# Kernel tuning notes

Measured on AMD Instinct MI355X. Metric: run time of the kernel, lower is better.

Reference implementation:

```python
import jax, jax.numpy as jnp
import numpy as np

B, S, D, H = 2, 2048, 1024, 16
HD = D // H  # 64


def setup_inputs() -> dict:
    key = jax.random.key(0)
    k0, k1, k2 = jax.random.split(key, 3)
    return {
        "x": jax.random.normal(k0, (B, S, D), jnp.float32),
        "qkv_w": jax.random.normal(k1, (D, 3 * D), jnp.float32) / np.sqrt(D).astype(np.float32),
        "qkv_b": jnp.zeros((3 * D,), jnp.float32),
        "out_w": jax.random.normal(k2, (D, D), jnp.float32) / np.sqrt(D).astype(np.float32),
        "out_b": jnp.zeros((D,), jnp.float32),
    }


def reference(x, qkv_w, qkv_b, out_w, out_b):
    b, s, d = x.shape
    h, hd = H, d // H
    scale = 1.0 / np.sqrt(hd).astype(np.float32)
    # qkv projection: [b, s, 3d] -> [b, s, 3, h, hd]
    qkv = (x @ qkv_w + qkv_b).reshape(b, s, 3, h, hd)
    q, k, v = qkv[:, :, 0], qkv[:, :, 1], qkv[:, :, 2]  # each [b, s, h, hd]
    # attention logits [b, h, q, k]
    logits = jnp.einsum("bqhd,bkhd->bhqk", q, k)
    # causal mask applied before scaling (as in source; -inf is scale-invariant)
    causal_mask = jnp.triu(jnp.ones((s, s), bool), 1)
    logits = jnp.where(causal_mask, -jnp.inf, logits) * scale
    att = jax.nn.softmax(logits, axis=-1)
    out = jnp.einsum("bhqk,bkhd->bqhd", att, v).reshape(b, s, d)
    return out @ out_w + out_b
```

## Files before the change

### kernel.cpp

```cpp
#include <hip/hip_runtime.h>


typedef __bf16 bf16x8 __attribute__((ext_vector_type(8)));
typedef float f32x4 __attribute__((ext_vector_type(4)));
typedef float f32x16 __attribute__((ext_vector_type(16)));
typedef unsigned short u16;
typedef u16 u16x8 __attribute__((ext_vector_type(8)));
typedef unsigned u32x4 __attribute__((ext_vector_type(4)));

#define NEG_INF (-__builtin_inff())
#define QSCALE 0.180336880110323f
#define FIXED_M 24.0f

__device__ __forceinline__ u16 f2b(float f) {
    unsigned u = __builtin_bit_cast(unsigned, f);
    u += 0x7fffu + ((u >> 16) & 1u);
    return (u16)(u >> 16);
}

__device__ __forceinline__ unsigned cvtpk(float lo, float hi) {
    unsigned r;
    asm("v_cvt_pk_bf16_f32 %0, %1, %2" : "=v"(r) : "v"(lo), "v"(hi));
    return r;
}

__device__ __forceinline__ void plswap(unsigned &a, unsigned &b) {
    asm("v_permlane32_swap_b32 %0, %1" : "+v"(a), "+v"(b));
}

__device__ __forceinline__ void gload_lds16(const u16* g, u16* l) {
    __builtin_amdgcn_global_load_lds(
        (__attribute__((address_space(1))) unsigned int*)(g),
        (__attribute__((address_space(3))) unsigned int*)(l),
        16u, 0, 0u);
}

__device__ __forceinline__ int swzb(int u) {
    return u ^ (((u >> 7) & 7) << 4);
}

__global__ void cast_f32_bf16(const float* __restrict__ X, u16* __restrict__ Y, int n4)
{
    int i = blockIdx.x * blockDim.x + threadIdx.x;
    if (i >= n4) return;
    float4 v = ((const float4*)X)[i];
    ((ushort4*)Y)[i] = make_ushort4(f2b(v.x), f2b(v.y), f2b(v.z), f2b(v.w));
}

__global__ void transpose_cast(const float* __restrict__ W, u16* __restrict__ Wt, int K, int N)
{
    __shared__ float tile[32][33];
    const int c0 = blockIdx.x * 32, r0 = blockIdx.y * 32;
    const int tc = threadIdx.x & 31, tr = threadIdx.x >> 5;
#pragma unroll
    for (int i = 0; i < 4; ++i)
        tile[tr + i*8][tc] = W[(size_t)(r0 + tr + i*8) * N + c0 + tc];
    __syncthreads();
#pragma unroll
    for (int i = 0; i < 4; ++i) {
        int nn = tr + i*8;
        Wt[(size_t)(c0 + nn) * K + r0 + tc] = f2b(tile[tc][nn]);
    }
}

template<int MODE>
__global__ __launch_bounds__(256) void gemm_bt(
    const u16* __restrict__ A, const u16* __restrict__ Bt,
    const float* __restrict__ bias, float* __restrict__ Cf,
    u16* __restrict__ qb, u16* __restrict__ kb, u16* __restrict__ vb,
    int M, int N, int K)
{
    __shared__ __align__(16) u16 As[2][128 * 32];
    __shared__ __align__(16) u16 Bs[2][128 * 32];
    const int tid  = threadIdx.x;
    const int wave = tid >> 6, lane = tid & 63;
    const int quad = lane >> 4, l16 = lane & 15;
    const int m0 = blockIdx.y * 128, n0 = blockIdx.x * 128;
    const int wm = (wave >> 1) * 64, wn = (wave & 1) * 64;

    f32x4 acc[4][4] = {};

    auto stage = [&](int buf, int kt) {
#pragma unroll
        for (int iss = 0; iss < 2; ++iss) {
            const int e = iss * 2048 + tid * 8;
            const int row = e >> 5, col = e & 31;
            gload_lds16(A  + (size_t)(m0 + row) * K + kt + col, &As[buf][iss * 2048 + wave * 512]);
            gload_lds16(Bt + (size_t)(n0 + row) * K + kt + col, &Bs[buf][iss * 2048 + wave * 512]);
        }
    };

    stage(0, 0);
    __syncthreads();

    int buf = 0;
    for (int kt = 0; kt < K; kt += 32) {
        if (kt + 32 < K) stage(buf ^ 1, kt + 32);

        bf16x8 af[4], bfr[4];
#pragma unroll
        for (int i = 0; i < 4; ++i) {
            af[i]  = *(const bf16x8*)(&As[buf][(wm + i*16 + l16) * 32 + quad * 8]);
            bfr[i] = *(const bf16x8*)(&Bs[buf][(wn + i*16 + l16) * 32 + quad * 8]);
        }
#pragma unroll
        for (int i = 0; i < 4; ++i)
#pragma unroll
            for (int j = 0; j < 4; ++j)
                acc[i][j] = __builtin_amdgcn_mfma_f32_16x16x32_bf16(af[i], bfr[j], acc[i][j], 0, 0, 0);
        __syncthreads();
        buf ^= 1;
    }

#pragma unroll
    for (int i = 0; i < 4; ++i)
#pragma unroll
        for (int j = 0; j < 4; ++j)
#pragma unroll
            for (int r = 0; r < 4; ++r) {
                const int m = m0 + wm + i*16 + quad*4 + r;
                const int n = n0 + wn + j*16 + l16;
                float v = acc[i][j][r] + bias[n];
                if (MODE == 0) {
                    Cf[(size_t)m * N + n] = v;
                } else {
                    const int t = n >> 10, h = (n >> 6) & 15, hd = n & 63;
                    const int b = m >> 11, s = m & 2047;
                    const size_t idx = ((size_t)(b * 16 + h) * 2048 + s) * 64 + hd;
                    if (t == 0)      qb[idx] = f2b(v * QSCALE);
                    else if (t == 1) kb[idx] = f2b(v);
                    else             vb[idx] = f2b(v);
                }
            }
}

__global__ __launch_bounds__(256) void transpose_v(const u16* __restrict__ vb, u16* __restrict__ vt)
{
    __shared__ u16 tile[64][72];
    const int bh = blockIdx.y, s0 = blockIdx.x * 64;
    const size_t base = (size_t)bh * (2048 * 64);
    const int r = threadIdx.x >> 3, c = (threadIdx.x & 7) * 8;
#pragma unroll
    for (int i = 0; i < 2; ++i) {
        u16x8 v = *(const u16x8*)(vb + base + (size_t)(s0 + r + i*32) * 64 + c);
        *(u16x8*)(&tile[r + i*32][c]) = v;
    }
    __syncthreads();
#pragma unroll
    for (int i = 0; i < 2; ++i) {
        const int hd = r + i*32;
        u16 tmp[8];
#pragma unroll
        for (int j = 0; j < 8; ++j) tmp[j] = tile[c + j][hd];
        *(u16x8*)(vt + base + (size_t)hd * 2048 + s0 + c) = *(u16x8*)&tmp[0];
    }
}

__global__ __launch_bounds__(256) void flash_attn(
    const u16* __restrict__ qb, const u16* __restrict__ kb, const u16* __restrict__ vt,
    u16* __restrict__ attn)
{
    __shared__ __align__(16) u16 Kl[2][4096];
    __shared__ __align__(16) u16 Vl[2][4096];
    __shared__ float red_f[2][2][2][16][64];
    __shared__ float red_li[2][2][64];
    __shared__ float al[2][2][32];

    const int tid  = threadIdx.x;
    const int wave = tid >> 6, lane = tid & 63;
    const int l31 = lane & 31, hi = lane >> 5;
    const int hi8 = hi * 8, hi4 = hi * 4;

    const int lin = (int)blockIdx.x;
    const int bh  = (lin & 7) | (((lin >> 3) & 3) << 3);
    const int g   = lin >> 5;
    const int pairsel = wave >> 1, phase = wave & 1;
    const int p   = 2 * g + pairsel;
    const size_t base = (size_t)bh * (2048 * 64);

    const int rb0 = 32 * p;
    const int rb1 = 32 * (63 - p);
    const int klo = p, khi = 63 - p;
    const int T = 32 - g;

    int koff[2], voff[2], dstw[2];
#pragma unroll
    for (int i = 0; i < 2; ++i) {
        const int u = (tid + 256 * i) * 16;
        const int ktsub = u >> 12, krow = (u >> 7) & 31;
        koff[i] = (ktsub * 32 + krow) * 64 + ((u & 127) >> 1);
        const int half = (u >> 6) & 1;
        voff[i] = (krow * 2 + half) * 2048 + ktsub * 32 + ((u & 63) >> 1);
        dstw[i] = swzb(u) >> 1;
    }
    int rdK[4], rdV[2][2];
#pragma unroll
    for (int ks = 0; ks < 4; ++ks) {
        const int u = phase * 4096 + l31 * 128 + ks * 32 + hi * 16;
        rdK[ks] = swzb(u) >> 1;
    }
#pragma unroll
    for (int c = 0; c < 2; ++c)
#pragma unroll
        for (int s2 = 0; s2 < 2; ++s2) {
            const int u = phase * 4096 + (c * 16 + (l31 >> 1)) * 128 + (l31 & 1) * 64
                        + s2 * 32 + hi * 16;
            rdV[c][s2] = swzb(u) >> 1;
        }

    bf16x8 qf[2][4];
#pragma unroll
    for (int ks = 0; ks < 4; ++ks) {
        qf[0][ks] = *(const bf16x8*)(qb + base + (size_t)(rb0 + l31) * 64 + ks*16 + hi8);
        qf[1][ks] = *(const bf16x8*)(qb + base + (size_t)(rb1 + l31) * 64 + ks*16 + hi8);
    }

    f32x16 minit;
#pragma unroll
    for (int r = 0; r < 16; ++r) minit[r] = -FIXED_M;

    f32x16 of[2][2] = {};
    float li[2] = {0.f, 0.f};

    u16x8 rk[2], rv[2];
    auto LOADS = [&](int s) {
#pragma unroll
        for (int i = 0; i < 2; ++i) {
            rk[i] = *(const u16x8*)(kb + base + (size_t)s * 4096 + koff[i]);
            rv[i] = *(const u16x8*)(vt + base + (size_t)s * 64 + voff[i]);
        }
    };
    auto WRITES = [&](int b) {
#pragma unroll
        for (int i = 0; i < 2; ++i) {
            *(u16x8*)(&Kl[b][dstw[i]]) = rk[i];
            *(u16x8*)(&Vl[b][dstw[i]]) = rv[i];
        }
    };

    LOADS(0); WRITES(0);
    __syncthreads();

    for (int s = 0; s < T; ++s) {
        const bool pre = (s + 1 < T);
        if (pre) LOADS(s + 1);

        const int kth = 2 * s + phase;
        const int key0 = kth * 32;
        const bool a_hi = (kth <= khi), a_lo = (kth <= klo);

        if (a_hi | a_lo) {
            const int buf = s & 1;
            bf16x8 kf[4], vf[2][2];
#pragma unroll
            for (int ks = 0; ks < 4; ++ks)
                kf[ks] = *(const bf16x8*)(&Kl[buf][rdK[ks]]);
#pragma unroll
            for (int c = 0; c < 2; ++c)
#pragma unroll
                for (int s2 = 0; s2 < 2; ++s2)
                    vf[c][s2] = *(const bf16x8*)(&Vl[buf][rdV[c][s2]]);

#define PROC_TILE(TT, RB, MT)                                                    \
        do {                                                                     \
            __builtin_amdgcn_s_setprio(1);                                       \
            f32x16 st = __builtin_amdgcn_mfma_f32_32x32x16_bf16(kf[0], qf[TT][0], minit, 0, 0, 0); \
            _Pragma("unroll")                                                    \
            for (int ks = 1; ks < 4; ++ks)                                       \
                st = __builtin_amdgcn_mfma_f32_32x32x16_bf16(kf[ks], qf[TT][ks], st, 0, 0, 0); \
            __builtin_amdgcn_s_setprio(0);                                       \
            const bool mt_ = (MT);                                               \
            const int lim_ = (RB) + l31 - key0;                                  \
            _Pragma("unroll")                                                    \
            for (int r = 0; r < 16; ++r) {                                       \
                float e = __builtin_exp2f(st[r]);                                \
                if (mt_ && ((r&3) + 8*(r>>2) + hi4 > lim_)) e = 0.f;             \
                st[r] = e;                                                       \
            }                                                                    \
            li[TT] += (((st[0]+st[1]) + (st[2]+st[3])) + ((st[4]+st[5]) + (st[6]+st[7]))) \
                    + (((st[8]+st[9]) + (st[10]+st[11])) + ((st[12]+st[13]) + (st[14]+st[15]))); \
            unsigned cw[8];                                                      \
            _Pragma("unroll")                                                    \
            for (int i = 0; i < 8; ++i) cw[i] = cvtpk(st[2*i], st[2*i+1]);       \
            plswap(cw[0], cw[2]); plswap(cw[1], cw[3]);                          \
            plswap(cw[4], cw[6]); plswap(cw[5], cw[7]);                          \
            bf16x8 pa[2];                                                        \
            { u32x4 t0 = {cw[0], cw[1], cw[2], cw[3]};                           \
              u32x4 t1 = {cw[4], cw[5], cw[6], cw[7]};                           \
              pa[0] = __builtin_bit_cast(bf16x8, t0);                            \
              pa[1] = __builtin_bit_cast(bf16x8, t1); }                          \
            __builtin_amdgcn_s_setprio(1);                                       \
            _Pragma("unroll")                                                    \
            for (int c = 0; c < 2; ++c) {                                        \
                of[TT][c] = __builtin_amdgcn_mfma_f32_32x32x16_bf16(pa[0], vf[c][0], of[TT][c], 0, 0, 0); \
                of[TT][c] = __builtin_amdgcn_mfma_f32_32x32x16_bf16(pa[1], vf[c][1], of[TT][c], 0, 0, 0); \
            }                                                                    \
            __builtin_amdgcn_s_setprio(0);                                       \
        } while (0)

            if (a_hi) PROC_TILE(1, rb1, kth == khi);
            if (a_lo) PROC_TILE(0, rb0, kth == klo);
#undef PROC_TILE
        }

        if (pre) WRITES((s + 1) & 1);
        __syncthreads();
    }

    if (phase) {
#pragma unroll
        for (int t = 0; t < 2; ++t) {
#pragma unroll
            for (int c = 0; c < 2; ++c)
#pragma unroll
                for (int i = 0; i < 16; ++i)
                    red_f[pairsel][t][c][i][lane] = of[t][c][i];
            red_li[pairsel][t][lane] = li[t];
        }
    }
    __syncthreads();
    if (phase) return;
#pragma unroll
    for (int t = 0; t < 2; ++t) {
#pragma unroll
        for (int c = 0; c < 2; ++c)
#pragma unroll
            for (int i = 0; i < 16; ++i)
                of[t][c][i] += red_f[pairsel][t][c][i][lane];
        li[t] += red_li[pairsel][t][lane];
    }

#pragma unroll
    for (int t = 0; t < 2; ++t) {
        li[t] += __shfl_xor(li[t], 32);
        al[pairsel][t][l31] = li[t];
    }
    const int b = bh >> 4, h = bh & 15;
    const int rbs[2] = {rb0, rb1};
#pragma unroll
    for (int t = 0; t < 2; ++t)
#pragma unroll
        for (int gq = 0; gq < 4; ++gq) {
            const f32x4 lv = *(const f32x4*)(&al[pairsel][t][gq*8 + hi4]);
            f32x4 inv;
#pragma unroll
            for (int rr = 0; rr < 4; ++rr) inv[rr] = 1.0f / lv[rr];
#pragma unroll
            for (int c = 0; c < 2; ++c)
#pragma unroll
                for (int rr = 0; rr < 4; ++rr) {
                    const int q = rbs[t] + gq*8 + hi4 + rr;
                    u16* dst = attn + ((size_t)(b * 2048 + q)) * 1024 + h * 64 + c*32;
                    dst[l31] = f2b(of[t][c][gq*4 + rr] * inv[rr]);
                }
        }
}

extern "C" void kernel_launch(void* const* d_in, const int* in_sizes, int n_in,
                              void* d_out, int out_size, void* d_ws, size_t ws_size,
                              hipStream_t stream)
{
    const float* x     = (const float*)d_in[0];
    const float* qkv_w = (const float*)d_in[1];
    const float* qkv_b = (const float*)d_in[2];
    const float* out_w = (const float*)d_in[3];
    const float* out_b = (const float*)d_in[4];
    float* out = (float*)d_out;

    char* ws = (char*)d_ws;
    u16* qkv_wt = (u16*)ws;  ws += (size_t)3072 * 1024 * 2;
    u16* out_wt = (u16*)ws;  ws += (size_t)1024 * 1024 * 2;
    u16* xb     = (u16*)ws;  ws += (size_t)4096 * 1024 * 2;
    u16* qb     = (u16*)ws;  ws += (size_t)4096 * 1024 * 2;
    u16* kb     = (u16*)ws;  ws += (size_t)4096 * 1024 * 2;
    u16* vb     = (u16*)ws;  ws += (size_t)4096 * 1024 * 2;
    u16* vt     = (u16*)ws;

    cast_f32_bf16<<<4096, 256, 0, stream>>>(x, xb, 4096 * 1024 / 4);
    transpose_cast<<<dim3(96, 32), 256, 0, stream>>>(qkv_w, qkv_wt, 1024, 3072);
    transpose_cast<<<dim3(32, 32), 256, 0, stream>>>(out_w, out_wt, 1024, 1024);

    gemm_bt<1><<<dim3(24, 32), 256, 0, stream>>>(xb, qkv_wt, qkv_b, nullptr,
                                                 qb, kb, vb, 4096, 3072, 1024);
    transpose_v<<<dim3(32, 32), 256, 0, stream>>>(vb, vt);
    flash_attn<<<512, 256, 0, stream>>>(qb, kb, vt, xb);
    gemm_bt<0><<<dim3(8, 32), 256, 0, stream>>>(xb, out_wt, out_b, out,
                                                nullptr, nullptr, nullptr, 4096, 1024, 1024);
}
```

Before: 196.6 us.

## Fuse V transpose into QKV GEMM epilogue and remap attention head order

The QKV GEMM epilogue now writes V straight into the transposed layout, staging it through shared memory that reuses the operand buffers. This removes the separate transpose_v kernel and the intermediate vb buffer, saving one launch and a full round trip of V through global memory. The flash attention block-to-head mapping is also reordered, likely to improve cache locality or load balance. The added epilogue needs extra syncthreads and LDS traffic in the V-column blocks.

```diff
diff --git a/kernel.cpp b/kernel.cpp
--- a/kernel.cpp
+++ b/kernel.cpp
@@ -67,11 +67,12 @@
 __global__ __launch_bounds__(256) void gemm_bt(
     const u16* __restrict__ A, const u16* __restrict__ Bt,
     const float* __restrict__ bias, float* __restrict__ Cf,
-    u16* __restrict__ qb, u16* __restrict__ kb, u16* __restrict__ vb,
+    u16* __restrict__ qb, u16* __restrict__ kb, u16* __restrict__ vt,
     int M, int N, int K)
 {
-    __shared__ __align__(16) u16 As[2][128 * 32];
-    __shared__ __align__(16) u16 Bs[2][128 * 32];
+    __shared__ __align__(16) u16 smem[16384];
+    u16* As = smem;
+    u16* Bs = smem + 8192;
     const int tid  = threadIdx.x;
     const int wave = tid >> 6, lane = tid & 63;
     const int quad = lane >> 4, l16 = lane & 15;
@@ -85,8 +86,8 @@
         for (int iss = 0; iss < 2; ++iss) {
             const int e = iss * 2048 + tid * 8;
             const int row = e >> 5, col = e & 31;
-            gload_lds16(A  + (size_t)(m0 + row) * K + kt + col, &As[buf][iss * 2048 + wave * 512]);
-            gload_lds16(Bt + (size_t)(n0 + row) * K + kt + col, &Bs[buf][iss * 2048 + wave * 512]);
+            gload_lds16(A  + (size_t)(m0 + row) * K + kt + col, As + buf*4096 + iss*2048 + wave*512);
+            gload_lds16(Bt + (size_t)(n0 + row) * K + kt + col, Bs + buf*4096 + iss*2048 + wave*512);
         }
     };
 
@@ -100,8 +101,8 @@
         bf16x8 af[4], bfr[4];
 #pragma unroll
         for (int i = 0; i < 4; ++i) {
-            af[i]  = *(const bf16x8*)(&As[buf][(wm + i*16 + l16) * 32 + quad * 8]);
-            bfr[i] = *(const bf16x8*)(&Bs[buf][(wn + i*16 + l16) * 32 + quad * 8]);
+            af[i]  = *(const bf16x8*)(As + buf*4096 + (wm + i*16 + l16) * 32 + quad * 8);
+            bfr[i] = *(const bf16x8*)(Bs + buf*4096 + (wn + i*16 + l16) * 32 + quad * 8);
         }
 #pragma unroll
         for (int i = 0; i < 4; ++i)
@@ -110,6 +111,41 @@
                 acc[i][j] = __builtin_amdgcn_mfma_f32_16x16x32_bf16(af[i], bfr[j], acc[i][j], 0, 0, 0);
         __syncthreads();
         buf ^= 1;
+    }
+
+    if (MODE == 1 && n0 >= 2048) {
+        const int b = m0 >> 11, s0 = m0 & 2047;
+        u16* TT = smem;
+#pragma unroll
+        for (int hh = 0; hh < 2; ++hh) {
+            if ((wave & 1) == hh) {
+#pragma unroll
+                for (int j = 0; j < 4; ++j) {
+                    const int hd = j*16 + l16;
+                    const float bv = bias[n0 + wn + j*16 + l16];
+#pragma unroll
+                    for (int i = 0; i < 4; ++i) {
+                        const int sl = wm + i*16 + quad*4;
+                        ushort4 w = make_ushort4(
+                            f2b(acc[i][j][0] + bv), f2b(acc[i][j][1] + bv),
+                            f2b(acc[i][j][2] + bv), f2b(acc[i][j][3] + bv));
+                        *(ushort4*)(&TT[hd*136 + sl]) = w;
+                    }
+                }
+            }
+            __syncthreads();
+            const int h = ((n0 + hh*64) >> 6) & 15;
+            u16* dst = vt + ((size_t)(b*16 + h)) * (64 * 2048) + s0;
+            const int rr = tid >> 4, cc = (tid & 15) * 8;
+#pragma unroll
+            for (int it = 0; it < 4; ++it) {
+                const int row = it*16 + rr;
+                u16x8 v = *(const u16x8*)(&TT[row*136 + cc]);
+                *(u16x8*)(dst + (size_t)row * 2048 + cc) = v;
+            }
+            __syncthreads();
+        }
+        return;
     }
 
 #pragma unroll
@@ -128,32 +164,9 @@
                     const int b = m >> 11, s = m & 2047;
                     const size_t idx = ((size_t)(b * 16 + h) * 2048 + s) * 64 + hd;
                     if (t == 0)      qb[idx] = f2b(v * QSCALE);
-                    else if (t == 1) kb[idx] = f2b(v);
-                    else             vb[idx] = f2b(v);
+                    else             kb[idx] = f2b(v);
                 }
             }
-}
-
-__global__ __launch_bounds__(256) void transpose_v(const u16* __restrict__ vb, u16* __restrict__ vt)
-{
-    __shared__ u16 tile[64][72];
-    const int bh = blockIdx.y, s0 = blockIdx.x * 64;
-    const size_t base = (size_t)bh * (2048 * 64);
-    const int r = threadIdx.x >> 3, c = (threadIdx.x & 7) * 8;
-#pragma unroll
-    for (int i = 0; i < 2; ++i) {
-        u16x8 v = *(const u16x8*)(vb + base + (size_t)(s0 + r + i*32) * 64 + c);
-        *(u16x8*)(&tile[r + i*32][c]) = v;
-    }
-    __syncthreads();
-#pragma unroll
-    for (int i = 0; i < 2; ++i) {
-        const int hd = r + i*32;
-        u16 tmp[8];
-#pragma unroll
-        for (int j = 0; j < 8; ++j) tmp[j] = tile[c + j][hd];
-        *(u16x8*)(vt + base + (size_t)hd * 2048 + s0 + c) = *(u16x8*)&tmp[0];
-    }
 }
 
 __global__ __launch_bounds__(256) void flash_attn(
@@ -172,7 +185,7 @@
     const int hi8 = hi * 8, hi4 = hi * 4;
 
     const int lin = (int)blockIdx.x;
-    const int bh  = (lin & 7) | (((lin >> 3) & 3) << 3);
+    const int bh  = 2*(lin & 7) + ((lin >> 3) & 1) + 16*((lin >> 4) & 1);
     const int g   = lin >> 5;
     const int pairsel = wave >> 1, phase = wave & 1;
     const int p   = 2 * g + pairsel;
@@ -373,7 +386,6 @@
     u16* xb     = (u16*)ws;  ws += (size_t)4096 * 1024 * 2;
     u16* qb     = (u16*)ws;  ws += (size_t)4096 * 1024 * 2;
     u16* kb     = (u16*)ws;  ws += (size_t)4096 * 1024 * 2;
-    u16* vb     = (u16*)ws;  ws += (size_t)4096 * 1024 * 2;
     u16* vt     = (u16*)ws;
 
     cast_f32_bf16<<<4096, 256, 0, stream>>>(x, xb, 4096 * 1024 / 4);
@@ -381,8 +393,7 @@
     transpose_cast<<<dim3(32, 32), 256, 0, stream>>>(out_w, out_wt, 1024, 1024);
 
     gemm_bt<1><<<dim3(24, 32), 256, 0, stream>>>(xb, qkv_wt, qkv_b, nullptr,
-                                                 qb, kb, vb, 4096, 3072, 1024);
-    transpose_v<<<dim3(32, 32), 256, 0, stream>>>(vb, vt);
+                                                 qb, kb, vt, 4096, 3072, 1024);
     flash_attn<<<512, 256, 0, stream>>>(qb, kb, vt, xb);
     gemm_bt<0><<<dim3(8, 32), 256, 0, stream>>>(xb, out_wt, out_b, out,
                                                 nullptr, nullptr, nullptr, 4096, 1024, 1024);
```

New measurement: 193.5 us. Within noise of the previous version (-1.5%).
